# Optimization experiments

Hardware: AMD Instinct MI355X
Metric: run time of the kernel (lower is better)

## Reference

```python
import jax, jax.numpy as jnp
import numpy as np

DIM = 2048
N_HEADS = 32
HEAD_DIM = DIM // N_HEADS
D_FF = 4 * DIM
EPS = 1e-5


def layernorm(x, g, b):
    mu = jnp.mean(x, axis=-1, keepdims=True)
    var = jnp.mean(jnp.square(x - mu), axis=-1, keepdims=True)
    return (x - mu) * jax.lax.rsqrt(var + EPS) * g + b


def setup_inputs() -> dict:
    key = jax.random.key(0)
    ks = jax.random.split(key, 12)
    s = 0.02
    # Linear weights stored as [in, out] (y = x @ W + b), equivalent math to torch's x @ W.T
    return {
        "x": jax.random.normal(ks[0], (2, 2048, DIM), jnp.float32),
        "w_qkv": jax.random.normal(ks[1], (DIM, 3 * DIM), jnp.float32) * s,
        "b_qkv": jnp.zeros((3 * DIM,), jnp.float32),
        "w_o": jax.random.normal(ks[2], (DIM, DIM), jnp.float32) * s,
        "b_o": jnp.zeros((DIM,), jnp.float32),
        "g1": jnp.ones((DIM,), jnp.float32),
        "beta1": jnp.zeros((DIM,), jnp.float32),
        "w1": jax.random.normal(ks[3], (DIM, D_FF), jnp.float32) * s,
        "b1": jnp.zeros((D_FF,), jnp.float32),
        "w2": jax.random.normal(ks[4], (D_FF, DIM), jnp.float32) * s,
        "b2": jnp.zeros((DIM,), jnp.float32),
        "g2": jnp.ones((DIM,), jnp.float32),
        "beta2": jnp.zeros((DIM,), jnp.float32),
    }


def reference(x, w_qkv, b_qkv, w_o, b_o, g1, beta1, w1, b1, w2, b2, g2, beta2):
    B, T, _ = x.shape
    residual = x
    h = layernorm(x, g1, beta1)
    qkv = h @ w_qkv + b_qkv                      # [B,T,3*DIM]
    qkv = qkv.reshape(B, T, 3, N_HEADS, HEAD_DIM)
    qkv = jnp.transpose(qkv, (2, 0, 3, 1, 4))    # [3,B,H,T,D]
    q, k, v = qkv[0], qkv[1], qkv[2]
    scores = jnp.einsum("bhtd,bhsd->bhts", q, k) / np.sqrt(HEAD_DIM).astype(np.float32)
    attn = jax.nn.softmax(scores, axis=-1)       # full T x T (non-causal), as in source
    out = jnp.einsum("bhts,bhsd->bhtd", attn, v)
    out = jnp.transpose(out, (0, 2, 1, 3)).reshape(B, T, DIM)
    h = out @ w_o + b_o
    x = h + residual
    residual = x
    h = layernorm(x, g2, beta2)
    h = jax.nn.gelu(h @ w1 + b1, approximate=False)  # torch nn.GELU default = exact erf
    h = h @ w2 + b2
    return h + residual
```

## Files before the change

kernel.cpp:

```cpp
#include <hip/hip_runtime.h>
#include <hip/hip_bf16.h>

#define DIM  2048
#define DFF  8192
#define NH   32
#define HD   64
#define TT   2048
#define MM   4096

typedef __attribute__((ext_vector_type(4))) float f32x4;
typedef __attribute__((ext_vector_type(4))) unsigned int u32x4;
typedef __attribute__((ext_vector_type(2))) unsigned int u32x2;
typedef unsigned short ushort_t;

#define MFMA16(ACC, A, B) \
  asm volatile("v_mfma_f32_16x16x32_bf16 %0, %1, %2, %0" : "+v"(ACC) : "v"(A), "v"(B))

#define GL16(GP, LP)                                                     \
  __builtin_amdgcn_global_load_lds(                                      \
      (const __attribute__((address_space(1))) void*)(GP),               \
      (__attribute__((address_space(3))) void*)(LP), 16, 0, 0)

__device__ __forceinline__ unsigned int f2bu(float f) {
  union { __hip_bfloat16 h; unsigned short u; } c;
  c.h = __float2bfloat16(f);
  return (unsigned int)c.u;
}

__global__ __launch_bounds__(256)
void transpose_cvt(const float* __restrict__ in, __hip_bfloat16* __restrict__ out,
                   int R, int C) {
  __shared__ float tile[32][33];
  const int tx = threadIdx.x, ty = threadIdx.y;
  const int bx = blockIdx.x * 32, by = blockIdx.y * 32;
#pragma unroll
  for (int i = 0; i < 32; i += 8)
    tile[ty + i][tx] = in[(size_t)(by + ty + i) * C + bx + tx];
  __syncthreads();
#pragma unroll
  for (int i = 0; i < 32; i += 8)
    out[(size_t)(bx + ty + i) * R + by + tx] = __float2bfloat16(tile[tx][ty + i]);
}

__global__ __launch_bounds__(256)
void ln_kernel(const float* __restrict__ in, const float* __restrict__ gw,
               const float* __restrict__ bw, __hip_bfloat16* __restrict__ out) {
  const int row = blockIdx.x;
  const int t = threadIdx.x;
  const float* x = in + (size_t)row * DIM;
  const float4 v0 = ((const float4*)x)[t * 2];
  const float4 v1 = ((const float4*)x)[t * 2 + 1];
  float s  = v0.x + v0.y + v0.z + v0.w + v1.x + v1.y + v1.z + v1.w;
  float ss = v0.x*v0.x + v0.y*v0.y + v0.z*v0.z + v0.w*v0.w
           + v1.x*v1.x + v1.y*v1.y + v1.z*v1.z + v1.w*v1.w;
#pragma unroll
  for (int o = 32; o >= 1; o >>= 1) { s += __shfl_xor(s, o); ss += __shfl_xor(ss, o); }
  __shared__ float red[8];
  if ((t & 63) == 0) { red[t >> 6] = s; red[4 + (t >> 6)] = ss; }
  __syncthreads();
  s  = red[0] + red[1] + red[2] + red[3];
  ss = red[4] + red[5] + red[6] + red[7];
  const float mean = s * (1.0f / DIM);
  const float rstd = rsqrtf(ss * (1.0f / DIM) - mean * mean + 1e-5f);
  const float4 g0 = ((const float4*)gw)[t * 2], g1 = ((const float4*)gw)[t * 2 + 1];
  const float4 b0 = ((const float4*)bw)[t * 2], b1 = ((const float4*)bw)[t * 2 + 1];
  uint4 o;
  o.x = f2bu((v0.x - mean) * rstd * g0.x + b0.x) | (f2bu((v0.y - mean) * rstd * g0.y + b0.y) << 16);
  o.y = f2bu((v0.z - mean) * rstd * g0.z + b0.z) | (f2bu((v0.w - mean) * rstd * g0.w + b0.w) << 16);
  o.z = f2bu((v1.x - mean) * rstd * g1.x + b1.x) | (f2bu((v1.y - mean) * rstd * g1.y + b1.y) << 16);
  o.w = f2bu((v1.z - mean) * rstd * g1.z + b1.z) | (f2bu((v1.w - mean) * rstd * g1.w + b1.w) << 16);
  *(uint4*)((char*)out + ((size_t)row * DIM + t * 8) * 2) = o;
}

template <int EPI>
__global__ __launch_bounds__(512, 2)
void gemm256(const __hip_bfloat16* __restrict__ Abf, const __hip_bfloat16* __restrict__ Btbf,
             const float* __restrict__ bias, const float* __restrict__ res,
             void* __restrict__ o0, void* __restrict__ o1, void* __restrict__ o2,
             int M, int N, int K, int nkt) {
  __shared__ ushort_t lds[2][2][16384];
  const int tid = threadIdx.x;
  const int l = tid & 63, w = tid >> 6;
  const int wm = w >> 2, wn = w & 3;
  const int g = l >> 4, q15 = l & 15;

  const int nby = M >> 8;
  const int nwg = (N >> 8) * nby;
  int id = blockIdx.x;
  {
    const int qq = nwg >> 3, rr = nwg & 7;
    const int xcd = id & 7, pos = id >> 3;
    id = (xcd < rr ? xcd * (qq + 1) : rr * (qq + 1) + (xcd - rr) * qq) + pos;
  }
  const int bm = (id % nby) << 8;
  const int bn = (id / nby) << 8;
  const int k0 = (EPI == 4) ? (int)blockIdx.y * (nkt << 6) : 0;

  const ushort_t* Au = (const ushort_t*)Abf;
  const ushort_t* Bu = (const ushort_t*)Btbf;
  const int sr = tid >> 3;
  const int sc = (((tid & 7) ^ (sr & 7)) << 3);
  const ushort_t* aBase = Au + (size_t)(bm + sr) * K + (k0 + sc);
  const ushort_t* bBase = Bu + (size_t)(bn + sr) * K + (k0 + sc);
  const int dOff = (w << 9) + (l << 3);

#define SA(buf, grp, kt_)                                                \
  GL16(aBase + (size_t)((grp) << 6) * K + ((kt_) << 6),                  \
       &lds[buf][0][((grp) << 12) + dOff])
#define SB(buf, grp, kt_)                                                \
  GL16(bBase + (size_t)((grp) << 6) * K + ((kt_) << 6),                  \
       &lds[buf][1][((grp) << 12) + dOff])

#define AFR(buf, m, ks)                                                        \
  (*(const u32x4*)&lds[buf][0][(((((m) & 4) << 5) + (wm << 6) +                \
                                 (((m) & 3) << 4) + q15) << 6) +               \
                               (((((ks) << 2) | g) ^ (q15 & 7)) << 3)])
#define BFR(buf, n, ks)                                                        \
  (*(const u32x4*)&lds[buf][1][((((wn) << 6) + ((n) << 4) + q15) << 6) +       \
                               (((((ks) << 2) | g) ^ (q15 & 7)) << 3)])

  f32x4 acc[8][4];
#pragma unroll
  for (int a = 0; a < 8; ++a)
#pragma unroll
    for (int b = 0; b < 4; ++b) acc[a][b] = (f32x4)0.0f;

  SB(0, 0, 0); SB(0, 1, 0); SB(0, 2, 0); SB(0, 3, 0);
  SA(0, 0, 0); SA(0, 1, 0); SA(0, 2, 0); SA(0, 3, 0);
  SB(1, 0, 1); SB(1, 1, 1); SB(1, 2, 1); SB(1, 3, 1);
  SA(1, 0, 1); SA(1, 1, 1);
  asm volatile("s_waitcnt vmcnt(8)" ::: "memory");
  __builtin_amdgcn_s_barrier();

  for (int kt = 0; kt < nkt; ++kt) {
    const int cur = kt & 1, oth = cur ^ 1;
    const bool p1 = (kt + 1) < nkt, p2 = (kt + 2) < nkt;
    u32x4 bf[4][2], af[2][2];

    if (p1) { SA(oth, 2, kt + 1); SA(oth, 3, kt + 1); }
#pragma unroll
    for (int n = 0; n < 4; ++n)
#pragma unroll
      for (int ks = 0; ks < 2; ++ks) bf[n][ks] = BFR(cur, n, ks);
#pragma unroll
    for (int mm = 0; mm < 2; ++mm)
#pragma unroll
      for (int ks = 0; ks < 2; ++ks) af[mm][ks] = AFR(cur, mm, ks);
    __builtin_amdgcn_s_barrier();
    asm volatile("s_waitcnt lgkmcnt(0)" ::: "memory");
    __builtin_amdgcn_s_setprio(1);
#pragma unroll
    for (int ks = 0; ks < 2; ++ks)
#pragma unroll
      for (int mm = 0; mm < 2; ++mm)
#pragma unroll
        for (int n = 0; n < 4; ++n) MFMA16(acc[mm][n], af[mm][ks], bf[n][ks]);
    __builtin_amdgcn_s_setprio(0);
    __builtin_amdgcn_s_barrier();

    if (p2) { SB(cur, 0, kt + 2); SB(cur, 1, kt + 2); }
#pragma unroll
    for (int mm = 0; mm < 2; ++mm)
#pragma unroll
      for (int ks = 0; ks < 2; ++ks) af[mm][ks] = AFR(cur, 2 + mm, ks);
    __builtin_amdgcn_s_barrier();
    asm volatile("s_waitcnt lgkmcnt(0)" ::: "memory");
    __builtin_amdgcn_s_setprio(1);
#pragma unroll
    for (int ks = 0; ks < 2; ++ks)
#pragma unroll
      for (int mm = 0; mm < 2; ++mm)
#pragma unroll
        for (int n = 0; n < 4; ++n) MFMA16(acc[2 + mm][n], af[mm][ks], bf[n][ks]);
    __builtin_amdgcn_s_setprio(0);
    if (p2)      asm volatile("s_waitcnt vmcnt(10)" ::: "memory");
    else if (p1) asm volatile("s_waitcnt vmcnt(8)"  ::: "memory");
    else         asm volatile("s_waitcnt vmcnt(0)"  ::: "memory");
    __builtin_amdgcn_s_barrier();

    if (p2) { SB(cur, 2, kt + 2); SB(cur, 3, kt + 2); }
#pragma unroll
    for (int mm = 0; mm < 2; ++mm)
#pragma unroll
      for (int ks = 0; ks < 2; ++ks) af[mm][ks] = AFR(cur, 4 + mm, ks);
    __builtin_amdgcn_s_barrier();
    asm volatile("s_waitcnt lgkmcnt(0)" ::: "memory");
    __builtin_amdgcn_s_setprio(1);
#pragma unroll
    for (int ks = 0; ks < 2; ++ks)
#pragma unroll
      for (int mm = 0; mm < 2; ++mm)
#pragma unroll
        for (int n = 0; n < 4; ++n) MFMA16(acc[4 + mm][n], af[mm][ks], bf[n][ks]);
    __builtin_amdgcn_s_setprio(0);
    __builtin_amdgcn_s_barrier();

    if (p2) { SA(cur, 0, kt + 2); SA(cur, 1, kt + 2); }
#pragma unroll
    for (int mm = 0; mm < 2; ++mm)
#pragma unroll
      for (int ks = 0; ks < 2; ++ks) af[mm][ks] = AFR(cur, 6 + mm, ks);
    __builtin_amdgcn_s_barrier();
    asm volatile("s_waitcnt lgkmcnt(0)" ::: "memory");
    __builtin_amdgcn_s_setprio(1);
#pragma unroll
    for (int ks = 0; ks < 2; ++ks)
#pragma unroll
      for (int mm = 0; mm < 2; ++mm)
#pragma unroll
        for (int n = 0; n < 4; ++n) MFMA16(acc[6 + mm][n], af[mm][ks], bf[n][ks]);
    __builtin_amdgcn_s_setprio(0);
    if (p2)      asm volatile("s_waitcnt vmcnt(8)" ::: "memory");
    else if (p1) asm volatile("s_waitcnt vmcnt(2)" ::: "memory");
    __builtin_amdgcn_s_barrier();
  }

#pragma unroll
  for (int m = 0; m < 8; ++m) {
    const int row0 = bm + ((m & 4) << 5) + (wm << 6) + ((m & 3) << 4) + (g << 2);
#pragma unroll
    for (int n = 0; n < 4; ++n) {
      const int col = bn + (wn << 6) + (n << 4) + q15;
      float bv = 0.0f;
      if constexpr (EPI != 4) bv = bias[col];
#pragma unroll
      for (int i = 0; i < 4; ++i) {
        const int mrow = row0 + i;
        float v = acc[m][n][i] + bv;
        if constexpr (EPI == 0) {
          const int sel = col >> 11, hd = col & 2047, h = hd >> 6, d = hd & 63;
          const int b = mrow >> 11, t = mrow & 2047;
          if (sel == 0) {
            ((__hip_bfloat16*)o0)[((size_t)(b * NH + h) * TT + t) * HD + d] =
                __float2bfloat16(v * 0.125f);
          } else if (sel == 1) {
            ((__hip_bfloat16*)o1)[((size_t)(b * NH + h) * TT + t) * HD + d] =
                __float2bfloat16(v);
          } else {
            ((__hip_bfloat16*)o2)[((size_t)(b * NH + h) * HD + d) * TT + t] =
                __float2bfloat16(v);
          }
        } else if constexpr (EPI == 2) {
          ((__hip_bfloat16*)o0)[(size_t)mrow * N + col] =
              __float2bfloat16(0.5f * v * (1.0f + erff(v * 0.70710678118654752f)));
        } else {
          ((float*)(blockIdx.y ? o1 : o0))[(size_t)mrow * N + col] = v;
        }
      }
    }
  }
#undef SA
#undef SB
#undef AFR
#undef BFR
}

__global__ __launch_bounds__(256)
void combine2(const float* __restrict__ p0, const float* __restrict__ p1,
              const float* __restrict__ bias, const float* __restrict__ res,
              float* __restrict__ out) {
  const size_t i = ((size_t)blockIdx.x * 256 + threadIdx.x) << 2;
  const float4 a = *(const float4*)(p0 + i);
  const float4 b = *(const float4*)(p1 + i);
  const float4 r = *(const float4*)(res + i);
  const float4 bi = *(const float4*)(bias + (i & (DIM - 1)));
  float4 o;
  o.x = a.x + b.x + r.x + bi.x;
  o.y = a.y + b.y + r.y + bi.y;
  o.z = a.z + b.z + r.z + bi.z;
  o.w = a.w + b.w + r.w + bi.w;
  *(float4*)(out + i) = o;
}

template <int EPI>
__global__ __launch_bounds__(256)
void gemm_bt(const __hip_bfloat16* __restrict__ A, const __hip_bfloat16* __restrict__ Bt,
             const float* __restrict__ bias, const float* __restrict__ res,
             void* __restrict__ o0, int M, int N, int K) {
  __shared__ __hip_bfloat16 As[128 * 32];
  __shared__ __hip_bfloat16 Bs[128 * 32];
  const int tid = threadIdx.x;
  const int l = tid & 63, w = tid >> 6;
  const int wr = w >> 1, wc = w & 1;
  const int g = l >> 4, q15 = l & 15;
  const int bm = blockIdx.y * 128, bn = blockIdx.x * 128;

  f32x4 acc[4][4];
#pragma unroll
  for (int a = 0; a < 4; ++a)
#pragma unroll
    for (int b = 0; b < 4; ++b) acc[a][b] = (f32x4)0.0f;

  const __hip_bfloat16* aSrc = A  + (size_t)(bm + (tid >> 2)) * K + (tid & 3) * 8;
  const __hip_bfloat16* bSrc = Bt + (size_t)(bn + (tid >> 2)) * K + (tid & 3) * 8;
  __hip_bfloat16* aDst = As + tid * 8;
  __hip_bfloat16* bDst = Bs + tid * 8;
  const size_t rowStep = (size_t)64 * K;

  for (int kt = 0; kt < K; kt += 32) {
    GL16(aSrc + kt,            aDst);
    GL16(aSrc + rowStep + kt,  aDst + 2048);
    GL16(bSrc + kt,            bDst);
    GL16(bSrc + rowStep + kt,  bDst + 2048);
    __syncthreads();
    u32x4 af[4], bf[4];
#pragma unroll
    for (int rb = 0; rb < 4; ++rb)
      af[rb] = *(const u32x4*)(As + (wr * 64 + rb * 16 + q15) * 32 + g * 8);
#pragma unroll
    for (int cb = 0; cb < 4; ++cb)
      bf[cb] = *(const u32x4*)(Bs + (wc * 64 + cb * 16 + q15) * 32 + g * 8);
#pragma unroll
    for (int rb = 0; rb < 4; ++rb)
#pragma unroll
      for (int cb = 0; cb < 4; ++cb) MFMA16(acc[rb][cb], af[rb], bf[cb]);
    __syncthreads();
  }

#pragma unroll
  for (int rb = 0; rb < 4; ++rb) {
    const int row0 = bm + wr * 64 + rb * 16 + g * 4;
#pragma unroll
    for (int cb = 0; cb < 4; ++cb) {
      const int col = bn + wc * 64 + cb * 16 + q15;
      const float bv = bias[col];
#pragma unroll
      for (int i = 0; i < 4; ++i) {
        const int m = row0 + i;
        float v = acc[rb][cb][i] + bv;
        ((float*)o0)[(size_t)m * N + col] = v + res[(size_t)m * N + col];
      }
    }
  }
}

__global__ __launch_bounds__(256)
void attn_kernel(const __hip_bfloat16* __restrict__ Q, const __hip_bfloat16* __restrict__ Kx,
                 const __hip_bfloat16* __restrict__ Vt, __hip_bfloat16* __restrict__ out) {
  __shared__ unsigned int Plds[4][2048];
  const int tid = threadIdx.x;
  const int l = tid & 63, w = tid >> 6;
  const int g = l >> 4, q15 = l & 15;
  const int bh = blockIdx.x >> 3;
  const int q0 = (blockIdx.x & 7) * 256 + w * 64;
  const __hip_bfloat16* Qb = Q  + (size_t)bh * TT * HD;
  const __hip_bfloat16* Kb = Kx + (size_t)bh * TT * HD;
  const __hip_bfloat16* Vb = Vt + (size_t)bh * HD * TT;
  unsigned int* Pw = Plds[w];

  u32x4 qf[4][2];
#pragma unroll
  for (int rb = 0; rb < 4; ++rb)
#pragma unroll
    for (int ks = 0; ks < 2; ++ks)
      qf[rb][ks] = *(const u32x4*)(Qb + (size_t)(q0 + rb * 16 + q15) * HD + ks * 32 + g * 8);

  f32x4 acc[4][4];
#pragma unroll
  for (int a = 0; a < 4; ++a)
#pragma unroll
    for (int b = 0; b < 4; ++b) acc[a][b] = (f32x4)0.0f;
  float mstat[4] = {-3e38f, -3e38f, -3e38f, -3e38f};
  float lstat[4] = {0.f, 0.f, 0.f, 0.f};

  for (int s0 = 0; s0 < TT; s0 += 64) {
    f32x4 st[4][4];
#pragma unroll
    for (int a = 0; a < 4; ++a)
#pragma unroll
      for (int b = 0; b < 4; ++b) st[a][b] = (f32x4)0.0f;
#pragma unroll
    for (int ks = 0; ks < 2; ++ks) {
      u32x4 kf[4];
#pragma unroll
      for (int cb = 0; cb < 4; ++cb)
        kf[cb] = *(const u32x4*)(Kb + (size_t)(s0 + cb * 16 + q15) * HD + ks * 32 + g * 8);
#pragma unroll
      for (int cb = 0; cb < 4; ++cb)
#pragma unroll
        for (int rb = 0; rb < 4; ++rb) MFMA16(st[cb][rb], kf[cb], qf[rb][ks]);
    }
#pragma unroll
    for (int rb = 0; rb < 4; ++rb) {
      float pm = st[0][rb][0];
#pragma unroll
      for (int cb = 0; cb < 4; ++cb)
#pragma unroll
        for (int i = 0; i < 4; ++i) pm = fmaxf(pm, st[cb][rb][i]);
      pm = fmaxf(pm, __shfl_xor(pm, 16));
      pm = fmaxf(pm, __shfl_xor(pm, 32));
      const float mnew = fmaxf(mstat[rb], pm);
      const float corr = __expf(mstat[rb] - mnew);
      mstat[rb] = mnew;
      float rs = 0.f;
#pragma unroll
      for (int cb = 0; cb < 4; ++cb)
#pragma unroll
        for (int i = 0; i < 4; ++i) {
          const float p = __expf(st[cb][rb][i] - mnew);
          st[cb][rb][i] = p;
          rs += p;
        }
      rs += __shfl_xor(rs, 16);
      rs += __shfl_xor(rs, 32);
      lstat[rb] = lstat[rb] * corr + rs;
#pragma unroll
      for (int db = 0; db < 4; ++db)
#pragma unroll
        for (int i = 0; i < 4; ++i) acc[db][rb][i] *= corr;
      const int row = rb * 16 + q15;
      const int rx = row & 7;
#pragma unroll
      for (int cb = 0; cb < 4; ++cb) {
        const unsigned int lo = f2bu(st[cb][rb][0]) | (f2bu(st[cb][rb][1]) << 16);
        const unsigned int hi = f2bu(st[cb][rb][2]) | (f2bu(st[cb][rb][3]) << 16);
        const int seg = (cb * 2 + (g >> 1)) ^ rx;
        u32x2 pk = {lo, hi};
        *(u32x2*)(Pw + row * 32 + seg * 4 + (g & 1) * 2) = pk;
      }
    }
#pragma unroll
    for (int ks2 = 0; ks2 < 2; ++ks2) {
      u32x4 vf[4], pf[4];
#pragma unroll
      for (int db = 0; db < 4; ++db)
        vf[db] = *(const u32x4*)(Vb + (size_t)(db * 16 + q15) * TT + s0 + ks2 * 32 + g * 8);
#pragma unroll
      for (int rb = 0; rb < 4; ++rb) {
        const int row = rb * 16 + q15;
        const int seg = (ks2 * 4 + g) ^ (row & 7);
        pf[rb] = *(const u32x4*)(Pw + row * 32 + seg * 4);
      }
#pragma unroll
      for (int db = 0; db < 4; ++db)
#pragma unroll
        for (int rb = 0; rb < 4; ++rb) MFMA16(acc[db][rb], vf[db], pf[rb]);
    }
  }
  const int b = bh >> 5, hh = bh & 31;
#pragma unroll
  for (int rb = 0; rb < 4; ++rb) {
    const float inv = 1.0f / lstat[rb];
    const size_t trow = (size_t)(b * TT + q0 + rb * 16 + q15);
#pragma unroll
    for (int db = 0; db < 4; ++db) {
      const unsigned int lo = f2bu(acc[db][rb][0] * inv) | (f2bu(acc[db][rb][1] * inv) << 16);
      const unsigned int hi = f2bu(acc[db][rb][2] * inv) | (f2bu(acc[db][rb][3] * inv) << 16);
      u32x2 pk = {lo, hi};
      *(u32x2*)(out + trow * DIM + hh * 64 + db * 16 + g * 4) = pk;
    }
  }
}

extern "C" void kernel_launch(void* const* d_in, const int* in_sizes, int n_in,
                              void* d_out, int out_size, void* d_ws, size_t ws_size,
                              hipStream_t stream) {
  (void)in_sizes; (void)n_in; (void)out_size; (void)ws_size;
  const float* x     = (const float*)d_in[0];
  const float* w_qkv = (const float*)d_in[1];
  const float* b_qkv = (const float*)d_in[2];
  const float* w_o   = (const float*)d_in[3];
  const float* b_o   = (const float*)d_in[4];
  const float* g1    = (const float*)d_in[5];
  const float* be1   = (const float*)d_in[6];
  const float* w1    = (const float*)d_in[7];
  const float* b1    = (const float*)d_in[8];
  const float* w2    = (const float*)d_in[9];
  const float* b2    = (const float*)d_in[10];
  const float* g2    = (const float*)d_in[11];
  const float* be2   = (const float*)d_in[12];

  char* ws = (char*)d_ws;
  size_t off = 0;
  auto alloc = [&](size_t bytes) {
    void* p = ws + off;
    off += (bytes + 255) & ~(size_t)255;
    return p;
  };
  __hip_bfloat16* WqkvT = (__hip_bfloat16*)alloc((size_t)6144 * 2048 * 2);
  __hip_bfloat16* WoT   = (__hip_bfloat16*)alloc((size_t)2048 * 2048 * 2);
  __hip_bfloat16* W1T   = (__hip_bfloat16*)alloc((size_t)8192 * 2048 * 2);
  __hip_bfloat16* W2T   = (__hip_bfloat16*)alloc((size_t)2048 * 8192 * 2);
  __hip_bfloat16* hbuf  = (__hip_bfloat16*)alloc((size_t)MM * DIM * 2);
  float*          xres  = (float*)alloc((size_t)MM * DIM * 4);
  __hip_bfloat16* Qb    = (__hip_bfloat16*)alloc((size_t)MM * DIM * 2);
  __hip_bfloat16* Kb    = (__hip_bfloat16*)alloc((size_t)MM * DIM * 2);
  __hip_bfloat16* Vtb   = (__hip_bfloat16*)alloc((size_t)MM * DIM * 2);
  __hip_bfloat16* attno = (__hip_bfloat16*)alloc((size_t)MM * DIM * 2);
  __hip_bfloat16* f1    = Qb;
  float* p0 = (float*)ws;
  float* p1 = (float*)(ws + (size_t)MM * DIM * 4);

  const dim3 tb(32, 8);
  transpose_cvt<<<dim3(6144 / 32, 2048 / 32), tb, 0, stream>>>(w_qkv, WqkvT, 2048, 6144);
  transpose_cvt<<<dim3(2048 / 32, 2048 / 32), tb, 0, stream>>>(w_o, WoT, 2048, 2048);
  transpose_cvt<<<dim3(8192 / 32, 2048 / 32), tb, 0, stream>>>(w1, W1T, 2048, 8192);
  transpose_cvt<<<dim3(2048 / 32, 8192 / 32), tb, 0, stream>>>(w2, W2T, 8192, 2048);

  ln_kernel<<<MM, 256, 0, stream>>>(x, g1, be1, hbuf);
  gemm256<0><<<dim3((6144 / 256) * (MM / 256)), 512, 0, stream>>>(
      hbuf, WqkvT, b_qkv, nullptr, Qb, Kb, Vtb, MM, 6144, 2048, 32);
  attn_kernel<<<512, 256, 0, stream>>>(Qb, Kb, Vtb, attno);
  gemm_bt<1><<<dim3(2048 / 128, MM / 128), 256, 0, stream>>>(
      attno, WoT, b_o, x, xres, MM, 2048, 2048);
  ln_kernel<<<MM, 256, 0, stream>>>(xres, g2, be2, hbuf);
  gemm256<2><<<dim3((8192 / 256) * (MM / 256)), 512, 0, stream>>>(
      hbuf, W1T, b1, nullptr, f1, nullptr, nullptr, MM, 8192, 2048, 32);
  gemm256<4><<<dim3((2048 / 256) * (MM / 256), 2), 512, 0, stream>>>(
      f1, W2T, nullptr, nullptr, p0, p1, nullptr, MM, 2048, 8192, 64);
  combine2<<<(MM * DIM) / 1024, 256, 0, stream>>>(p0, p1, b2, xres, (float*)d_out);
}
```

Before: 772.9 us.

## Unroll GEMM main loop by two with precomputed LDS addresses and AGPR accumulators

Rewrites the bf16 GEMM main loop as a two-iteration unrolled body so the double-buffer index becomes a compile-time constant. LDS fragment reads now go through inline ds_read_b128 calls with precomputed base addresses and immediate offsets, which removes per-iteration address arithmetic. Accumulators are bound to AGPRs in the MFMA asm, and sched_barrier pins the instruction order. The loop assumes nkt is at least 2, and the fixed asm constraints may force extra register moves or reduce occupancy.

```diff
diff --git a/kernel.cpp b/kernel.cpp
--- a/kernel.cpp
+++ b/kernel.cpp
@@ -15,11 +15,23 @@
 
 #define MFMA16(ACC, A, B) \
   asm volatile("v_mfma_f32_16x16x32_bf16 %0, %1, %2, %0" : "+v"(ACC) : "v"(A), "v"(B))
+#define MFMA16A(ACC, A, B) \
+  asm volatile("v_mfma_f32_16x16x32_bf16 %0, %1, %2, %0" : "+a"(ACC) : "v"(A), "v"(B))
 
 #define GL16(GP, LP)                                                     \
   __builtin_amdgcn_global_load_lds(                                      \
       (const __attribute__((address_space(1))) void*)(GP),               \
       (__attribute__((address_space(3))) void*)(LP), 16, 0, 0)
+
+#define VM(N) asm volatile("s_waitcnt vmcnt(" #N ")" ::: "memory")
+#define NOOP  ((void)0)
+
+template <int IMM>
+__device__ __forceinline__ u32x4 dsr(unsigned a) {
+  u32x4 d;
+  asm volatile("ds_read_b128 %0, %1 offset:%2" : "=v"(d) : "v"(a), "i"(IMM));
+  return d;
+}
 
 __device__ __forceinline__ unsigned int f2bu(float f) {
   union { __hip_bfloat16 h; unsigned short u; } c;
@@ -104,116 +116,115 @@
   const ushort_t* bBase = Bu + (size_t)(bn + sr) * K + (k0 + sc);
   const int dOff = (w << 9) + (l << 3);
 
-#define SA(buf, grp, kt_)                                                \
-  GL16(aBase + (size_t)((grp) << 6) * K + ((kt_) << 6),                  \
-       &lds[buf][0][((grp) << 12) + dOff])
-#define SB(buf, grp, kt_)                                                \
-  GL16(bBase + (size_t)((grp) << 6) * K + ((kt_) << 6),                  \
-       &lds[buf][1][((grp) << 12) + dOff])
-
-#define AFR(buf, m, ks)                                                        \
-  (*(const u32x4*)&lds[buf][0][(((((m) & 4) << 5) + (wm << 6) +                \
-                                 (((m) & 3) << 4) + q15) << 6) +               \
-                               (((((ks) << 2) | g) ^ (q15 & 7)) << 3)])
-#define BFR(buf, n, ks)                                                        \
-  (*(const u32x4*)&lds[buf][1][((((wn) << 6) + ((n) << 4) + q15) << 6) +       \
-                               (((((ks) << 2) | g) ^ (q15 & 7)) << 3)])
+#define SA(BUF, GRP, KT_)                                                \
+  GL16(aBase + (size_t)((GRP) << 6) * K + ((KT_) << 6),                  \
+       &lds[BUF][0][((GRP) << 12) + dOff])
+#define SB(BUF, GRP, KT_)                                                \
+  GL16(bBase + (size_t)((GRP) << 6) * K + ((KT_) << 6),                  \
+       &lds[BUF][1][((GRP) << 12) + dOff])
+
+  const unsigned lbase =
+      (unsigned)(size_t)(__attribute__((address_space(3))) ushort_t*)&lds[0][0][0];
+  const int x7 = q15 & 7;
+  const unsigned laneA = (unsigned)(q15 * 128);
+  const unsigned c0 = (unsigned)((g ^ x7) * 16);
+  const unsigned c1 = (unsigned)(((4 | g) ^ x7) * 16);
+  const unsigned aAk0b0 = lbase + wm * 8192 + laneA + c0;
+  const unsigned aAk1b0 = lbase + wm * 8192 + laneA + c1;
+  const unsigned aAk0b1 = aAk0b0 + 65536;
+  const unsigned aAk1b1 = aAk1b0 + 65536;
+  const unsigned aBk0b0 = lbase + 32768 + wn * 8192 + laneA + c0;
+  const unsigned aBk1b0 = lbase + 32768 + wn * 8192 + laneA + c1;
+  const unsigned aBk0b1 = aBk0b0 + 65536;
+  const unsigned aBk1b1 = aBk1b0 + 65536;
+
+#define AOFFC(M) (((M) & 4) * 4096 + ((M) & 3) * 2048)
+#define RDA(BUF, M0, M1) do{                                             \
+    af[0][0] = dsr<AOFFC(M0)>(aAk0b##BUF);                               \
+    af[0][1] = dsr<AOFFC(M0)>(aAk1b##BUF);                               \
+    af[1][0] = dsr<AOFFC(M1)>(aAk0b##BUF);                               \
+    af[1][1] = dsr<AOFFC(M1)>(aAk1b##BUF); }while(0)
+#define RDB(BUF) do{                                                     \
+    bf[0][0] = dsr<0>(aBk0b##BUF);    bf[0][1] = dsr<0>(aBk1b##BUF);     \
+    bf[1][0] = dsr<2048>(aBk0b##BUF); bf[1][1] = dsr<2048>(aBk1b##BUF);  \
+    bf[2][0] = dsr<4096>(aBk0b##BUF); bf[2][1] = dsr<4096>(aBk1b##BUF);  \
+    bf[3][0] = dsr<6144>(aBk0b##BUF); bf[3][1] = dsr<6144>(aBk1b##BUF); }while(0)
+
+#define LGK0 do{ asm volatile("s_waitcnt lgkmcnt(0)" ::: "memory");      \
+                 __builtin_amdgcn_sched_barrier(0); }while(0)
+
+#define CLUSTER(R0, R1) do{                                              \
+    __builtin_amdgcn_s_setprio(1);                                       \
+    MFMA16A(acc[R0][0], af[0][0], bf[0][0]);                             \
+    MFMA16A(acc[R0][1], af[0][0], bf[1][0]);                             \
+    MFMA16A(acc[R0][2], af[0][0], bf[2][0]);                             \
+    MFMA16A(acc[R0][3], af[0][0], bf[3][0]);                             \
+    MFMA16A(acc[R1][0], af[1][0], bf[0][0]);                             \
+    MFMA16A(acc[R1][1], af[1][0], bf[1][0]);                             \
+    MFMA16A(acc[R1][2], af[1][0], bf[2][0]);                             \
+    MFMA16A(acc[R1][3], af[1][0], bf[3][0]);                             \
+    MFMA16A(acc[R0][0], af[0][1], bf[0][1]);                             \
+    MFMA16A(acc[R0][1], af[0][1], bf[1][1]);                             \
+    MFMA16A(acc[R0][2], af[0][1], bf[2][1]);                             \
+    MFMA16A(acc[R0][3], af[0][1], bf[3][1]);                             \
+    MFMA16A(acc[R1][0], af[1][1], bf[0][1]);                             \
+    MFMA16A(acc[R1][1], af[1][1], bf[1][1]);                             \
+    MFMA16A(acc[R1][2], af[1][1], bf[2][1]);                             \
+    MFMA16A(acc[R1][3], af[1][1], bf[3][1]);                             \
+    __builtin_amdgcn_s_setprio(0); }while(0)
+
+#define HALF(BUF, OBUF, ktA23, PFA, ktN, PFN, W1C, W3C)                  \
+  do {                                                                   \
+                                               \
+    if (PFA) { SA(OBUF, 2, ktA23); SA(OBUF, 3, ktA23); }                 \
+    RDB(BUF); RDA(BUF, 0, 1);                                            \
+    __builtin_amdgcn_s_barrier();                                        \
+    LGK0; CLUSTER(0, 1);                                                 \
+    __builtin_amdgcn_s_barrier();                                        \
+                                                       \
+    if (PFN) { SB(BUF, 0, ktN); SB(BUF, 1, ktN); }                       \
+    RDA(BUF, 2, 3);                                                      \
+    __builtin_amdgcn_s_barrier();                                        \
+    LGK0; CLUSTER(2, 3);                                                 \
+    W1C;                                                                 \
+    __builtin_amdgcn_s_barrier();                                        \
+                                                       \
+    if (PFN) { SB(BUF, 2, ktN); SB(BUF, 3, ktN); }                       \
+    RDA(BUF, 4, 5);                                                      \
+    __builtin_amdgcn_s_barrier();                                        \
+    LGK0; CLUSTER(4, 5);                                                 \
+    __builtin_amdgcn_s_barrier();                                        \
+                                                       \
+    if (PFN) { SA(BUF, 0, ktN); SA(BUF, 1, ktN); }                       \
+    RDA(BUF, 6, 7);                                                      \
+    __builtin_amdgcn_s_barrier();                                        \
+    LGK0; CLUSTER(6, 7);                                                 \
+    W3C;                                                                 \
+    __builtin_amdgcn_s_barrier();                                        \
+  } while (0)
 
   f32x4 acc[8][4];
 #pragma unroll
   for (int a = 0; a < 8; ++a)
 #pragma unroll
     for (int b = 0; b < 4; ++b) acc[a][b] = (f32x4)0.0f;
+
+  u32x4 bf[4][2], af[2][2];
 
   SB(0, 0, 0); SB(0, 1, 0); SB(0, 2, 0); SB(0, 3, 0);
   SA(0, 0, 0); SA(0, 1, 0); SA(0, 2, 0); SA(0, 3, 0);
   SB(1, 0, 1); SB(1, 1, 1); SB(1, 2, 1); SB(1, 3, 1);
   SA(1, 0, 1); SA(1, 1, 1);
-  asm volatile("s_waitcnt vmcnt(8)" ::: "memory");
+  VM(8);
   __builtin_amdgcn_s_barrier();
 
-  for (int kt = 0; kt < nkt; ++kt) {
-    const int cur = kt & 1, oth = cur ^ 1;
-    const bool p1 = (kt + 1) < nkt, p2 = (kt + 2) < nkt;
-    u32x4 bf[4][2], af[2][2];
-
-    if (p1) { SA(oth, 2, kt + 1); SA(oth, 3, kt + 1); }
-#pragma unroll
-    for (int n = 0; n < 4; ++n)
-#pragma unroll
-      for (int ks = 0; ks < 2; ++ks) bf[n][ks] = BFR(cur, n, ks);
-#pragma unroll
-    for (int mm = 0; mm < 2; ++mm)
-#pragma unroll
-      for (int ks = 0; ks < 2; ++ks) af[mm][ks] = AFR(cur, mm, ks);
-    __builtin_amdgcn_s_barrier();
-    asm volatile("s_waitcnt lgkmcnt(0)" ::: "memory");
-    __builtin_amdgcn_s_setprio(1);
-#pragma unroll
-    for (int ks = 0; ks < 2; ++ks)
-#pragma unroll
-      for (int mm = 0; mm < 2; ++mm)
-#pragma unroll
-        for (int n = 0; n < 4; ++n) MFMA16(acc[mm][n], af[mm][ks], bf[n][ks]);
-    __builtin_amdgcn_s_setprio(0);
-    __builtin_amdgcn_s_barrier();
-
-    if (p2) { SB(cur, 0, kt + 2); SB(cur, 1, kt + 2); }
-#pragma unroll
-    for (int mm = 0; mm < 2; ++mm)
-#pragma unroll
-      for (int ks = 0; ks < 2; ++ks) af[mm][ks] = AFR(cur, 2 + mm, ks);
-    __builtin_amdgcn_s_barrier();
-    asm volatile("s_waitcnt lgkmcnt(0)" ::: "memory");
-    __builtin_amdgcn_s_setprio(1);
-#pragma unroll
-    for (int ks = 0; ks < 2; ++ks)
-#pragma unroll
-      for (int mm = 0; mm < 2; ++mm)
-#pragma unroll
-        for (int n = 0; n < 4; ++n) MFMA16(acc[2 + mm][n], af[mm][ks], bf[n][ks]);
-    __builtin_amdgcn_s_setprio(0);
-    if (p2)      asm volatile("s_waitcnt vmcnt(10)" ::: "memory");
-    else if (p1) asm volatile("s_waitcnt vmcnt(8)"  ::: "memory");
-    else         asm volatile("s_waitcnt vmcnt(0)"  ::: "memory");
-    __builtin_amdgcn_s_barrier();
-
-    if (p2) { SB(cur, 2, kt + 2); SB(cur, 3, kt + 2); }
-#pragma unroll
-    for (int mm = 0; mm < 2; ++mm)
-#pragma unroll
-      for (int ks = 0; ks < 2; ++ks) af[mm][ks] = AFR(cur, 4 + mm, ks);
-    __builtin_amdgcn_s_barrier();
-    asm volatile("s_waitcnt lgkmcnt(0)" ::: "memory");
-    __builtin_amdgcn_s_setprio(1);
-#pragma unroll
-    for (int ks = 0; ks < 2; ++ks)
-#pragma unroll
-      for (int mm = 0; mm < 2; ++mm)
-#pragma unroll
-        for (int n = 0; n < 4; ++n) MFMA16(acc[4 + mm][n], af[mm][ks], bf[n][ks]);
-    __builtin_amdgcn_s_setprio(0);
-    __builtin_amdgcn_s_barrier();
-
-    if (p2) { SA(cur, 0, kt + 2); SA(cur, 1, kt + 2); }
-#pragma unroll
-    for (int mm = 0; mm < 2; ++mm)
-#pragma unroll
-      for (int ks = 0; ks < 2; ++ks) af[mm][ks] = AFR(cur, 6 + mm, ks);
-    __builtin_amdgcn_s_barrier();
-    asm volatile("s_waitcnt lgkmcnt(0)" ::: "memory");
-    __builtin_amdgcn_s_setprio(1);
-#pragma unroll
-    for (int ks = 0; ks < 2; ++ks)
-#pragma unroll
-      for (int mm = 0; mm < 2; ++mm)
-#pragma unroll
-        for (int n = 0; n < 4; ++n) MFMA16(acc[6 + mm][n], af[mm][ks], bf[n][ks]);
-    __builtin_amdgcn_s_setprio(0);
-    if (p2)      asm volatile("s_waitcnt vmcnt(8)" ::: "memory");
-    else if (p1) asm volatile("s_waitcnt vmcnt(2)" ::: "memory");
-    __builtin_amdgcn_s_barrier();
-  }
+  int kt = 0;
+  for (; kt + 3 < nkt; kt += 2) {
+    HALF(0, 1, kt + 1, true, kt + 2, true, VM(10), VM(8));
+    HALF(1, 0, kt + 2, true, kt + 3, true, VM(10), VM(8));
+  }
+  HALF(0, 1, kt + 1, true,  kt + 2, false, VM(8), VM(2));
+  HALF(1, 0, kt + 2, false, kt + 3, false, VM(0), NOOP);
 
 #pragma unroll
   for (int m = 0; m < 8; ++m) {
@@ -251,8 +262,12 @@
   }
 #undef SA
 #undef SB
-#undef AFR
-#undef BFR
+#undef RDA
+#undef RDB
+#undef HALF
+#undef CLUSTER
+#undef LGK0
+#undef AOFFC
 }
 
 __global__ __launch_bounds__(256)
```

Result: faster. 757.2 us (-2.0%).
